# Kernel tuning notes

Hardware: AMD Instinct MI355X
Metric: run time of the kernel (lower is better)

Reference implementation:

```python
import jax, jax.numpy as jnp
import numpy as np

N_HEAD = 16  # matches init_kwargs


def _rope_cos_sin(T, head_dim):
    # inv_freq over even indices, as in AdvancedRotaryEmbedding
    inv_freq = 1.0 / (10000.0 ** (jnp.arange(0, head_dim, 2, dtype=jnp.float32) / head_dim))
    t = jnp.arange(T, dtype=jnp.float32)
    freqs = t[:, None] * inv_freq[None, :]  # [T, head_dim/2]
    return jnp.cos(freqs), jnp.sin(freqs)


def _apply_rope(x, cos, sin):
    # x: [B, H, T, D]; cos/sin: [T, D/2] (broadcast over B, H)
    x1, x2 = x[..., 0::2], x[..., 1::2]
    # half-concat layout, faithful to the module's apply_rotary_emb
    return jnp.concatenate([x1 * cos - x2 * sin, x1 * sin + x2 * cos], axis=-1)


def reference(x, Wq, Wk, Wv, Wo):
    B, T, C = x.shape
    H = N_HEAD
    D = C // H
    # QKV projections (torch Linear: y = x @ W.T), then split heads -> [B, H, T, D]
    q = (x @ Wq.T).reshape(B, T, H, D).transpose(0, 2, 1, 3)
    k = (x @ Wk.T).reshape(B, T, H, D).transpose(0, 2, 1, 3)
    v = (x @ Wv.T).reshape(B, T, H, D).transpose(0, 2, 1, 3)
    cos, sin = _rope_cos_sin(T, D)
    cos = cos.astype(x.dtype)
    sin = sin.astype(x.dtype)
    q = _apply_rope(q, cos, sin)
    k = _apply_rope(k, cos, sin)
    # causal SDPA (eval mode -> dropout_p = 0); jax.nn expects [B, T, H, D]
    y = jax.nn.dot_product_attention(
        q.transpose(0, 2, 1, 3),
        k.transpose(0, 2, 1, 3),
        v.transpose(0, 2, 1, 3),
        is_causal=True,
    )  # [B, T, H, D]
    y = y.reshape(B, T, C)
    return y @ Wo.T


def setup_inputs() -> dict:
    key = jax.random.key(0)
    ks = jax.random.split(key, 5)
    B, T, C = 2, 2048, 1024
    s = 1.0 / np.sqrt(C)
    return {
        "x": jax.random.normal(ks[0], (B, T, C), dtype=jnp.float32),
        "Wq": jax.random.normal(ks[1], (C, C), dtype=jnp.float32) * s,
        "Wk": jax.random.normal(ks[2], (C, C), dtype=jnp.float32) * s,
        "Wv": jax.random.normal(ks[3], (C, C), dtype=jnp.float32) * s,
        "Wo": jax.random.normal(ks[4], (C, C), dtype=jnp.float32) * s,
    }
```

## Files before the change

kernel.cpp:

```cpp
#include <hip/hip_runtime.h>
#include <cstdint>
#include <cstddef>

typedef short s16x8 __attribute__((ext_vector_type(8)));
typedef float f32x4 __attribute__((ext_vector_type(4)));

#define MFMA16(a, b, c) __builtin_amdgcn_mfma_f32_16x16x32_bf16((a), (b), (c), 0, 0, 0)

constexpr int LDP = 72;

__device__ __forceinline__ short f2bf(float f) {
    unsigned u = __builtin_bit_cast(unsigned, f);
    u += 0x7FFFu + ((u >> 16) & 1u);
    return (short)(u >> 16);
}
__device__ __forceinline__ float bf2f(short s) {
    unsigned u = ((unsigned)(unsigned short)s) << 16;
    return __builtin_bit_cast(float, u);
}
__device__ __forceinline__ unsigned pack2(float a, float b) {
    return (unsigned)(unsigned short)f2bf(a) | ((unsigned)(unsigned short)f2bf(b) << 16);
}

__device__ __forceinline__ void async_ld16(const void* g, void* l) {
    __builtin_amdgcn_global_load_lds(
        (const __attribute__((address_space(1))) unsigned int*)g,
        (__attribute__((address_space(3))) unsigned int*)l, 16, 0, 0);
}

__global__ __launch_bounds__(256) void convert_kernel(
    const float* __restrict__ x, const float* __restrict__ Wq,
    const float* __restrict__ Wk, const float* __restrict__ Wv,
    const float* __restrict__ Wo, short* __restrict__ xb, short* __restrict__ wb) {
    const size_t f = ((size_t)blockIdx.x * 256 + threadIdx.x) * 8;
    const float* src;
    short* dst;
    if (f < 4194304) { src = x + f; dst = xb + f; }
    else {
        size_t wo = f - 4194304;
        int seg = (int)(wo >> 20);
        const float* ws4[4] = {Wq, Wk, Wv, Wo};
        src = ws4[seg] + (wo & 1048575u);
        dst = wb + wo;
    }
    float4 a = ((const float4*)src)[0];
    float4 b = ((const float4*)src)[1];
    *(uint4*)dst = make_uint4(pack2(a.x, a.y), pack2(a.z, a.w),
                              pack2(b.x, b.y), pack2(b.z, b.w));
}

__global__ __launch_bounds__(256) void qkv_kernel(
    const short* __restrict__ xb, const short* __restrict__ wb,
    short* __restrict__ Qo, short* __restrict__ Ko, short* __restrict__ VTo) {
    __shared__ __align__(16) short sA[128 * 64];
    __shared__ __align__(16) short sB[128 * 64];
    const int tid = threadIdx.x;
    const int w = tid >> 6, lane = tid & 63, quad = lane >> 4, l15 = lane & 15;
    const int wm = w & 1, wn = w >> 1;
    const int bx = blockIdx.x, by = blockIdx.y;
    const int m0 = by * 128;
    const int nb = bx * 128;

    f32x4 acc[4][4];
#pragma unroll
    for (int i = 0; i < 4; i++)
#pragma unroll
        for (int j = 0; j < 4; j++) acc[i][j] = f32x4{0.f, 0.f, 0.f, 0.f};

    for (int kb = 0; kb < 16; kb++) {
        const int k0 = kb * 64;
        if (kb) __syncthreads();
#pragma unroll
        for (int i = 0; i < 4; i++) {
            int c = i * 256 + tid;
            int row = c >> 3, col8 = (c & 7) * 8;
            async_ld16(xb + (size_t)(m0 + row) * 1024 + k0 + col8,
                       &sA[(i * 256 + w * 64) * 8]);
            async_ld16(wb + (size_t)(nb + row) * 1024 + k0 + col8,
                       &sB[(i * 256 + w * 64) * 8]);
        }
        __syncthreads();
#pragma unroll
        for (int ks = 0; ks < 2; ks++) {
            s16x8 av[4], bv[4];
#pragma unroll
            for (int at = 0; at < 4; at++)
                av[at] = *(const s16x8*)&sA[(wm * 64 + at * 16 + l15) * 64 + ks * 32 + quad * 8];
#pragma unroll
            for (int bt = 0; bt < 4; bt++)
                bv[bt] = *(const s16x8*)&sB[(wn * 64 + bt * 16 + l15) * 64 + ks * 32 + quad * 8];
#pragma unroll
            for (int at = 0; at < 4; at++)
#pragma unroll
                for (int bt = 0; bt < 4; bt++)
                    acc[at][bt] = MFMA16(av[at], bv[bt], acc[at][bt]);
        }
    }

    const int wsel = bx >> 3;
    const int h = (bx & 7) * 2 + wn;
    if (wsel == 2) {
#pragma unroll
        for (int at = 0; at < 4; at++) {
            int m = m0 + wm * 64 + at * 16 + quad * 4;
            int b = m >> 11, t0 = m & 2047;
            size_t base = ((size_t)((b * 16 + h) * 64)) * 2048;
#pragma unroll
            for (int bt = 0; bt < 4; bt++) {
                int d = bt * 16 + l15;
                unsigned lo = pack2(acc[at][bt][0], acc[at][bt][1]);
                unsigned hi = pack2(acc[at][bt][2], acc[at][bt][3]);
                *(uint2*)&VTo[base + (size_t)d * 2048 + t0] = make_uint2(lo, hi);
            }
        }
    } else {
        short* Out = (wsel == 0) ? Qo : Ko;
#pragma unroll
        for (int at = 0; at < 4; at++)
#pragma unroll
            for (int r = 0; r < 4; r++) {
                int m = m0 + wm * 64 + at * 16 + quad * 4 + r;
                int b = m >> 11, t = m & 2047;
                size_t base = (((size_t)(b * 16 + h)) * 2048 + t) * 64;
#pragma unroll
                for (int bt = 0; bt < 4; bt++)
                    Out[base + bt * 16 + l15] = f2bf(acc[at][bt][r]);
            }
    }
}

__global__ __launch_bounds__(256) void rope_kernel(short* __restrict__ Q, short* __restrict__ K) {
    const int rid = blockIdx.x * 256 + threadIdx.x;
    const bool isK = (rid & 65536) != 0;
    short* buf = isK ? K : Q;
    const float sc = isK ? 1.0f : 0.18033688011112042f;
    const int r2 = rid & 65535;
    const int t = r2 & 2047;
    short* row = buf + (size_t)r2 * 64;

    unsigned wv[32];
    const uint4* rp = (const uint4*)row;
#pragma unroll
    for (int c = 0; c < 8; c++) {
        uint4 v = rp[c];
        wv[c * 4 + 0] = v.x; wv[c * 4 + 1] = v.y; wv[c * 4 + 2] = v.z; wv[c * 4 + 3] = v.w;
    }
    float y1[32], y2[32];
    const float tf = (float)t;
#pragma unroll
    for (int i = 0; i < 32; i++) {
        float x1 = bf2f((short)(wv[i] & 0xFFFFu));
        float x2 = bf2f((short)(wv[i] >> 16));
        float inv = expf(-9.2103403719761836f * (float)i * (1.0f / 32.0f));
        float fr = tf * inv;
        float sn, cs;
        sincosf(fr, &sn, &cs);
        y1[i] = (x1 * cs - x2 * sn) * sc;
        y2[i] = (x1 * sn + x2 * cs) * sc;
    }
    unsigned ow[32];
#pragma unroll
    for (int i = 0; i < 16; i++) ow[i] = pack2(y1[2 * i], y1[2 * i + 1]);
#pragma unroll
    for (int i = 0; i < 16; i++) ow[16 + i] = pack2(y2[2 * i], y2[2 * i + 1]);
    uint4* wp = (uint4*)row;
#pragma unroll
    for (int c = 0; c < 8; c++)
        wp[c] = make_uint4(ow[c * 4 + 0], ow[c * 4 + 1], ow[c * 4 + 2], ow[c * 4 + 3]);
}

__global__ __launch_bounds__(256) void attn_kernel(
    const short* __restrict__ Q, const short* __restrict__ K,
    const short* __restrict__ VT, short* __restrict__ Y) {
    __shared__ __align__(16) short sQP[64 * LDP];
    __shared__ __align__(16) short sK[64 * LDP];
    __shared__ __align__(16) short sVT[64 * LDP];

    const int tid = threadIdx.x;
    const int w = tid >> 6, lane = tid & 63, quad = lane >> 4, l15 = lane & 15;
    const int px = blockIdx.x;
    const int bh = blockIdx.y;
    const int b = bh >> 4, h = bh & 15;
    const short* Qp = Q + (size_t)bh * 2048 * 64;
    const short* Kp = K + (size_t)bh * 2048 * 64;
    const short* Vp = VT + (size_t)bh * 64 * 2048;

    for (int pass = 0; pass < 2; pass++) {
        const int qt = pass ? (31 - px) : px;
        __syncthreads();
#pragma unroll
        for (int i = 0; i < 2; i++) {
            int p = tid + i * 256;
            int row = p >> 3, c8 = p & 7;
            uint4 v = *(const uint4*)(Qp + (size_t)(qt * 64 + row) * 64 + c8 * 8);
            *(uint4*)&sQP[row * LDP + c8 * 8] = v;
        }
        __syncthreads();
        s16x8 aq[2];
#pragma unroll
        for (int ks = 0; ks < 2; ks++)
            aq[ks] = *(const s16x8*)&sQP[(w * 16 + l15) * LDP + ks * 32 + quad * 8];

        f32x4 o[4];
#pragma unroll
        for (int i = 0; i < 4; i++) o[i] = f32x4{0.f, 0.f, 0.f, 0.f};
        float mrun = -INFINITY;
        float lrun = 0.f;
        const int q_idx = qt * 64 + w * 16 + l15;

        for (int kt = 0; kt <= qt; kt++) {
            __syncthreads();
#pragma unroll
            for (int i = 0; i < 2; i++) {
                int p = tid + i * 256;
                int row = p >> 3, c8 = p & 7;
                uint4 kv = *(const uint4*)(Kp + (size_t)(kt * 64 + row) * 64 + c8 * 8);
                *(uint4*)&sK[row * LDP + c8 * 8] = kv;
                uint4 vv = *(const uint4*)(Vp + (size_t)row * 2048 + kt * 64 + c8 * 8);
                *(uint4*)&sVT[row * LDP + c8 * 8] = vv;
            }
            __syncthreads();

            f32x4 sa[4];
#pragma unroll
            for (int i = 0; i < 4; i++) sa[i] = f32x4{0.f, 0.f, 0.f, 0.f};
#pragma unroll
            for (int ks = 0; ks < 2; ks++) {
#pragma unroll
                for (int ct = 0; ct < 4; ct++) {
                    s16x8 kf = *(const s16x8*)&sK[(ct * 16 + l15) * LDP + ks * 32 + quad * 8];
                    sa[ct] = MFMA16(kf, aq[ks], sa[ct]);
                }
            }

            const bool diag = (kt == qt);
            float ps[4][4];
#pragma unroll
            for (int ct = 0; ct < 4; ct++) {
                int kbase = kt * 64 + ct * 16 + quad * 4;
#pragma unroll
                for (int r = 0; r < 4; r++) {
                    float s = sa[ct][r];
                    if (diag && (kbase + r) > q_idx) s = -INFINITY;
                    ps[ct][r] = s;
                }
            }
            float cm[4];
#pragma unroll
            for (int ct = 0; ct < 4; ct++)
                cm[ct] = fmaxf(fmaxf(ps[ct][0], ps[ct][1]), fmaxf(ps[ct][2], ps[ct][3]));
            float mx = fmaxf(fmaxf(cm[0], cm[1]), fmaxf(cm[2], cm[3]));
            mx = fmaxf(mx, __shfl_xor(mx, 16));
            mx = fmaxf(mx, __shfl_xor(mx, 32));
            float mnew = fmaxf(mrun, mx);
            float alpha = exp2f(mrun - mnew);
            mrun = mnew;
            float cs[4];
#pragma unroll
            for (int ct = 0; ct < 4; ct++) {
#pragma unroll
                for (int r = 0; r < 4; r++) ps[ct][r] = exp2f(ps[ct][r] - mnew);
                cs[ct] = (ps[ct][0] + ps[ct][1]) + (ps[ct][2] + ps[ct][3]);
            }
            float psum = (cs[0] + cs[1]) + (cs[2] + cs[3]);
            psum += __shfl_xor(psum, 16);
            psum += __shfl_xor(psum, 32);
            lrun = lrun * alpha + psum;

            float arow[4];
#pragma unroll
            for (int r = 0; r < 4; r++) arow[r] = __shfl(alpha, quad * 4 + r);
#pragma unroll
            for (int ct = 0; ct < 4; ct++)
#pragma unroll
                for (int r = 0; r < 4; r++) o[ct][r] *= arow[r];

#pragma unroll
            for (int ct = 0; ct < 4; ct++) {
                unsigned lo = pack2(ps[ct][0], ps[ct][1]);
                unsigned hi = pack2(ps[ct][2], ps[ct][3]);
                *(uint2*)&sQP[(w * 16 + l15) * LDP + ct * 16 + quad * 4] = make_uint2(lo, hi);
            }

#pragma unroll
            for (int ks2 = 0; ks2 < 2; ks2++) {
                s16x8 pa = *(const s16x8*)&sQP[(w * 16 + l15) * LDP + ks2 * 32 + quad * 8];
#pragma unroll
                for (int ct = 0; ct < 4; ct++) {
                    s16x8 vb = *(const s16x8*)&sVT[(ct * 16 + l15) * LDP + ks2 * 32 + quad * 8];
                    o[ct] = MFMA16(pa, vb, o[ct]);
                }
            }
        }

#pragma unroll
        for (int r = 0; r < 4; r++) {
            float linv = 1.0f / __shfl(lrun, quad * 4 + r);
            int t = qt * 64 + w * 16 + quad * 4 + r;
#pragma unroll
            for (int ct = 0; ct < 4; ct++) {
                float val = o[ct][r] * linv;
                Y[((size_t)(b * 2048 + t)) * 1024 + h * 64 + ct * 16 + l15] = f2bf(val);
            }
        }
    }
}

__global__ __launch_bounds__(256) void oproj_kernel(
    const short* __restrict__ Yb, const short* __restrict__ Wob, float* __restrict__ out) {
    __shared__ __align__(16) short sA[128 * 64];
    __shared__ __align__(16) short sB[128 * 64];
    const int tid = threadIdx.x;
    const int w = tid >> 6, lane = tid & 63, quad = lane >> 4, l15 = lane & 15;
    const int wm = w & 1, wn = w >> 1;
    const int m0 = blockIdx.y * 128;
    const int nb = blockIdx.x * 128;

    f32x4 acc[4][4];
#pragma unroll
    for (int i = 0; i < 4; i++)
#pragma unroll
        for (int j = 0; j < 4; j++) acc[i][j] = f32x4{0.f, 0.f, 0.f, 0.f};

    for (int kb = 0; kb < 16; kb++) {
        const int k0 = kb * 64;
        if (kb) __syncthreads();
#pragma unroll
        for (int i = 0; i < 4; i++) {
            int c = i * 256 + tid;
            int row = c >> 3, col8 = (c & 7) * 8;
            async_ld16(Yb + (size_t)(m0 + row) * 1024 + k0 + col8,
                       &sA[(i * 256 + w * 64) * 8]);
            async_ld16(Wob + (size_t)(nb + row) * 1024 + k0 + col8,
                       &sB[(i * 256 + w * 64) * 8]);
        }
        __syncthreads();
#pragma unroll
        for (int ks = 0; ks < 2; ks++) {
            s16x8 av[4], bv[4];
#pragma unroll
            for (int at = 0; at < 4; at++)
                av[at] = *(const s16x8*)&sA[(wm * 64 + at * 16 + l15) * 64 + ks * 32 + quad * 8];
#pragma unroll
            for (int bt = 0; bt < 4; bt++)
                bv[bt] = *(const s16x8*)&sB[(wn * 64 + bt * 16 + l15) * 64 + ks * 32 + quad * 8];
#pragma unroll
            for (int at = 0; at < 4; at++)
#pragma unroll
                for (int bt = 0; bt < 4; bt++)
                    acc[at][bt] = MFMA16(av[at], bv[bt], acc[at][bt]);
        }
    }
#pragma unroll
    for (int at = 0; at < 4; at++)
#pragma unroll
        for (int r = 0; r < 4; r++) {
            int m = m0 + wm * 64 + at * 16 + quad * 4 + r;
#pragma unroll
            for (int bt = 0; bt < 4; bt++) {
                int n = nb + wn * 64 + bt * 16 + l15;
                out[(size_t)m * 1024 + n] = acc[at][bt][r];
            }
        }
}

extern "C" void kernel_launch(void* const* d_in, const int* in_sizes, int n_in,
                              void* d_out, int out_size, void* d_ws, size_t ws_size,
                              hipStream_t stream) {
    (void)in_sizes; (void)n_in; (void)out_size; (void)ws_size;
    const float* x  = (const float*)d_in[0];
    const float* Wq = (const float*)d_in[1];
    const float* Wk = (const float*)d_in[2];
    const float* Wv = (const float*)d_in[3];
    const float* Wo = (const float*)d_in[4];
    float* out = (float*)d_out;

    const size_t NE = (size_t)2 * 16 * 2048 * 64;
    short* Q  = (short*)d_ws;
    short* K  = Q + NE;
    short* VT = K + NE;
    short* Y  = VT + NE;
    short* xb = Y;
    short* wb = Y + NE;

    convert_kernel<<<4096, 256, 0, stream>>>(x, Wq, Wk, Wv, Wo, xb, wb);
    qkv_kernel<<<dim3(24, 32), 256, 0, stream>>>(xb, wb, Q, K, VT);
    rope_kernel<<<512, 256, 0, stream>>>(Q, K);
    attn_kernel<<<dim3(16, 32), 256, 0, stream>>>(Q, K, VT, Y);
    oproj_kernel<<<dim3(8, 32), 256, 0, stream>>>(Y, wb + 3 * 1048576, out);
}
```

Baseline: 237.3 us.

## Split causal attention KV range into chunks with a separate combine kernel

Attention work is split so each block handles one query tile over a chunk of up to eight key tiles. The grid grows from 512 to 2560 blocks, ordered longest-first. Each block writes an unnormalized partial output plus its running max and sum, and a new combine kernel merges them with log-sum-exp rescaling. This is meant to raise occupancy and balance on the many CUs, at the cost of an extra kernel launch and partial-result traffic. The P-to-bf16 pack also switches to truncation instead of round-to-nearest.

Result: faster. 217.7 us (-8.2%).

```diff
diff --git a/kernel.cpp b/kernel.cpp
--- a/kernel.cpp
+++ b/kernel.cpp
@@ -20,6 +20,11 @@
 }
 __device__ __forceinline__ unsigned pack2(float a, float b) {
     return (unsigned)(unsigned short)f2bf(a) | ((unsigned)(unsigned short)f2bf(b) << 16);
+}
+__device__ __forceinline__ unsigned pack2t(float a, float b) {
+    unsigned ua = __builtin_bit_cast(unsigned, a);
+    unsigned ub = __builtin_bit_cast(unsigned, b);
+    return (ua >> 16) | (ub & 0xFFFF0000u);
 }
 
 __device__ __forceinline__ void async_ld16(const void* g, void* l) {
@@ -171,139 +176,198 @@
 
 __global__ __launch_bounds__(256) void attn_kernel(
     const short* __restrict__ Q, const short* __restrict__ K,
-    const short* __restrict__ VT, short* __restrict__ Y) {
+    const short* __restrict__ VT, short* __restrict__ paO, float* __restrict__ ml) {
     __shared__ __align__(16) short sQP[64 * LDP];
     __shared__ __align__(16) short sK[64 * LDP];
     __shared__ __align__(16) short sVT[64 * LDP];
 
     const int tid = threadIdx.x;
     const int w = tid >> 6, lane = tid & 63, quad = lane >> 4, l15 = lane & 15;
-    const int px = blockIdx.x;
+    const int u = 79 - blockIdx.x;
     const int bh = blockIdx.y;
-    const int b = bh >> 4, h = bh & 15;
+
+    int qt, c;
+    if (u < 8)       { qt = u; c = 0; }
+    else if (u < 24) { int v = u - 8;  qt = 8 + (v >> 1); c = v & 1; }
+    else if (u < 48) { int v = u - 24; qt = 16 + v / 3;   c = v - 3 * (qt - 16); }
+    else             { int v = u - 48; qt = 24 + (v >> 2); c = v & 3; }
+    const int kt0 = c * 8;
+    const int kt1 = min(kt0 + 7, qt);
+
     const short* Qp = Q + (size_t)bh * 2048 * 64;
     const short* Kp = K + (size_t)bh * 2048 * 64;
     const short* Vp = VT + (size_t)bh * 64 * 2048;
 
-    for (int pass = 0; pass < 2; pass++) {
-        const int qt = pass ? (31 - px) : px;
+#pragma unroll
+    for (int i = 0; i < 2; i++) {
+        int p = tid + i * 256;
+        int row = p >> 3, c8 = p & 7;
+        uint4 v = *(const uint4*)(Qp + (size_t)(qt * 64 + row) * 64 + c8 * 8);
+        *(uint4*)&sQP[row * LDP + c8 * 8] = v;
+    }
+    __syncthreads();
+    s16x8 aq[2];
+#pragma unroll
+    for (int ks = 0; ks < 2; ks++)
+        aq[ks] = *(const s16x8*)&sQP[(w * 16 + l15) * LDP + ks * 32 + quad * 8];
+
+    f32x4 o[4];
+#pragma unroll
+    for (int i = 0; i < 4; i++) o[i] = f32x4{0.f, 0.f, 0.f, 0.f};
+    float mrun = -INFINITY;
+    float lrun = 0.f;
+    const int q_idx = qt * 64 + w * 16 + l15;
+
+    for (int kt = kt0; kt <= kt1; kt++) {
         __syncthreads();
 #pragma unroll
         for (int i = 0; i < 2; i++) {
             int p = tid + i * 256;
             int row = p >> 3, c8 = p & 7;
-            uint4 v = *(const uint4*)(Qp + (size_t)(qt * 64 + row) * 64 + c8 * 8);
-            *(uint4*)&sQP[row * LDP + c8 * 8] = v;
+            uint4 kv = *(const uint4*)(Kp + (size_t)(kt * 64 + row) * 64 + c8 * 8);
+            *(uint4*)&sK[row * LDP + c8 * 8] = kv;
+            uint4 vv = *(const uint4*)(Vp + (size_t)row * 2048 + kt * 64 + c8 * 8);
+            *(uint4*)&sVT[row * LDP + c8 * 8] = vv;
         }
         __syncthreads();
-        s16x8 aq[2];
-#pragma unroll
-        for (int ks = 0; ks < 2; ks++)
-            aq[ks] = *(const s16x8*)&sQP[(w * 16 + l15) * LDP + ks * 32 + quad * 8];
-
-        f32x4 o[4];
-#pragma unroll
-        for (int i = 0; i < 4; i++) o[i] = f32x4{0.f, 0.f, 0.f, 0.f};
-        float mrun = -INFINITY;
-        float lrun = 0.f;
-        const int q_idx = qt * 64 + w * 16 + l15;
-
-        for (int kt = 0; kt <= qt; kt++) {
-            __syncthreads();
-#pragma unroll
-            for (int i = 0; i < 2; i++) {
-                int p = tid + i * 256;
-                int row = p >> 3, c8 = p & 7;
-                uint4 kv = *(const uint4*)(Kp + (size_t)(kt * 64 + row) * 64 + c8 * 8);
-                *(uint4*)&sK[row * LDP + c8 * 8] = kv;
-                uint4 vv = *(const uint4*)(Vp + (size_t)row * 2048 + kt * 64 + c8 * 8);
-                *(uint4*)&sVT[row * LDP + c8 * 8] = vv;
-            }
-            __syncthreads();
-
-            f32x4 sa[4];
-#pragma unroll
-            for (int i = 0; i < 4; i++) sa[i] = f32x4{0.f, 0.f, 0.f, 0.f};
-#pragma unroll
-            for (int ks = 0; ks < 2; ks++) {
-#pragma unroll
-                for (int ct = 0; ct < 4; ct++) {
-                    s16x8 kf = *(const s16x8*)&sK[(ct * 16 + l15) * LDP + ks * 32 + quad * 8];
-                    sa[ct] = MFMA16(kf, aq[ks], sa[ct]);
-                }
-            }
-
-            const bool diag = (kt == qt);
-            float ps[4][4];
+
+        f32x4 sa[4];
+#pragma unroll
+        for (int i = 0; i < 4; i++) sa[i] = f32x4{0.f, 0.f, 0.f, 0.f};
+#pragma unroll
+        for (int ks = 0; ks < 2; ks++) {
 #pragma unroll
             for (int ct = 0; ct < 4; ct++) {
-                int kbase = kt * 64 + ct * 16 + quad * 4;
-#pragma unroll
-                for (int r = 0; r < 4; r++) {
-                    float s = sa[ct][r];
-                    if (diag && (kbase + r) > q_idx) s = -INFINITY;
-                    ps[ct][r] = s;
-                }
-            }
-            float cm[4];
-#pragma unroll
-            for (int ct = 0; ct < 4; ct++)
-                cm[ct] = fmaxf(fmaxf(ps[ct][0], ps[ct][1]), fmaxf(ps[ct][2], ps[ct][3]));
-            float mx = fmaxf(fmaxf(cm[0], cm[1]), fmaxf(cm[2], cm[3]));
-            mx = fmaxf(mx, __shfl_xor(mx, 16));
-            mx = fmaxf(mx, __shfl_xor(mx, 32));
-            float mnew = fmaxf(mrun, mx);
-            float alpha = exp2f(mrun - mnew);
-            mrun = mnew;
-            float cs[4];
+                s16x8 kf = *(const s16x8*)&sK[(ct * 16 + l15) * LDP + ks * 32 + quad * 8];
+                sa[ct] = MFMA16(kf, aq[ks], sa[ct]);
+            }
+        }
+
+        const bool diag = (kt == qt);
+        float ps[4][4];
+#pragma unroll
+        for (int ct = 0; ct < 4; ct++) {
+            int kbase = kt * 64 + ct * 16 + quad * 4;
+#pragma unroll
+            for (int r = 0; r < 4; r++) {
+                float s = sa[ct][r];
+                if (diag && (kbase + r) > q_idx) s = -INFINITY;
+                ps[ct][r] = s;
+            }
+        }
+        float cm[4];
+#pragma unroll
+        for (int ct = 0; ct < 4; ct++)
+            cm[ct] = fmaxf(fmaxf(ps[ct][0], ps[ct][1]), fmaxf(ps[ct][2], ps[ct][3]));
+        float mx = fmaxf(fmaxf(cm[0], cm[1]), fmaxf(cm[2], cm[3]));
+        mx = fmaxf(mx, __shfl_xor(mx, 16));
+        mx = fmaxf(mx, __shfl_xor(mx, 32));
+        float mnew = fmaxf(mrun, mx);
+        float alpha = exp2f(mrun - mnew);
+        mrun = mnew;
+        float cs[4];
+#pragma unroll
+        for (int ct = 0; ct < 4; ct++) {
+#pragma unroll
+            for (int r = 0; r < 4; r++) ps[ct][r] = exp2f(ps[ct][r] - mnew);
+            cs[ct] = (ps[ct][0] + ps[ct][1]) + (ps[ct][2] + ps[ct][3]);
+        }
+        float psum = (cs[0] + cs[1]) + (cs[2] + cs[3]);
+        psum += __shfl_xor(psum, 16);
+        psum += __shfl_xor(psum, 32);
+        lrun = lrun * alpha + psum;
+
+        float arow[4];
+#pragma unroll
+        for (int r = 0; r < 4; r++) arow[r] = __shfl(alpha, quad * 4 + r);
+#pragma unroll
+        for (int ct = 0; ct < 4; ct++)
+#pragma unroll
+            for (int r = 0; r < 4; r++) o[ct][r] *= arow[r];
+
+#pragma unroll
+        for (int ct = 0; ct < 4; ct++) {
+            unsigned lo = pack2t(ps[ct][0], ps[ct][1]);
+            unsigned hi = pack2t(ps[ct][2], ps[ct][3]);
+            *(uint2*)&sQP[(w * 16 + l15) * LDP + ct * 16 + quad * 4] = make_uint2(lo, hi);
+        }
+
+#pragma unroll
+        for (int ks2 = 0; ks2 < 2; ks2++) {
+            s16x8 pa = *(const s16x8*)&sQP[(w * 16 + l15) * LDP + ks2 * 32 + quad * 8];
 #pragma unroll
             for (int ct = 0; ct < 4; ct++) {
-#pragma unroll
-                for (int r = 0; r < 4; r++) ps[ct][r] = exp2f(ps[ct][r] - mnew);
-                cs[ct] = (ps[ct][0] + ps[ct][1]) + (ps[ct][2] + ps[ct][3]);
-            }
-            float psum = (cs[0] + cs[1]) + (cs[2] + cs[3]);
-            psum += __shfl_xor(psum, 16);
-            psum += __shfl_xor(psum, 32);
-            lrun = lrun * alpha + psum;
-
-            float arow[4];
-#pragma unroll
-            for (int r = 0; r < 4; r++) arow[r] = __shfl(alpha, quad * 4 + r);
-#pragma unroll
-            for (int ct = 0; ct < 4; ct++)
-#pragma unroll
-                for (int r = 0; r < 4; r++) o[ct][r] *= arow[r];
-
-#pragma unroll
-            for (int ct = 0; ct < 4; ct++) {
-                unsigned lo = pack2(ps[ct][0], ps[ct][1]);
-                unsigned hi = pack2(ps[ct][2], ps[ct][3]);
-                *(uint2*)&sQP[(w * 16 + l15) * LDP + ct * 16 + quad * 4] = make_uint2(lo, hi);
-            }
-
-#pragma unroll
-            for (int ks2 = 0; ks2 < 2; ks2++) {
-                s16x8 pa = *(const s16x8*)&sQP[(w * 16 + l15) * LDP + ks2 * 32 + quad * 8];
-#pragma unroll
-                for (int ct = 0; ct < 4; ct++) {
-                    s16x8 vb = *(const s16x8*)&sVT[(ct * 16 + l15) * LDP + ks2 * 32 + quad * 8];
-                    o[ct] = MFMA16(pa, vb, o[ct]);
-                }
-            }
-        }
-
-#pragma unroll
-        for (int r = 0; r < 4; r++) {
-            float linv = 1.0f / __shfl(lrun, quad * 4 + r);
-            int t = qt * 64 + w * 16 + quad * 4 + r;
-#pragma unroll
-            for (int ct = 0; ct < 4; ct++) {
-                float val = o[ct][r] * linv;
-                Y[((size_t)(b * 2048 + t)) * 1024 + h * 64 + ct * 16 + l15] = f2bf(val);
-            }
-        }
-    }
+                s16x8 vb = *(const s16x8*)&sVT[(ct * 16 + l15) * LDP + ks2 * 32 + quad * 8];
+                o[ct] = MFMA16(pa, vb, o[ct]);
+            }
+        }
+    }
+
+    const size_t pbase = ((size_t)(bh * 80 + u)) * 4096;
+#pragma unroll
+    for (int r = 0; r < 4; r++) {
+        int row = w * 16 + quad * 4 + r;
+#pragma unroll
+        for (int ct = 0; ct < 4; ct++)
+            paO[pbase + row * 64 + ct * 16 + l15] = f2bf(o[ct][r]);
+    }
+    if (quad == 0) {
+        int mlbase = (bh * 80 + u) * 128;
+        ml[mlbase + w * 16 + l15] = mrun;
+        ml[mlbase + 64 + w * 16 + l15] = lrun;
+    }
+}
+
+__global__ __launch_bounds__(256) void combine_kernel(
+    const short* __restrict__ paO, const float* __restrict__ ml, short* __restrict__ Y) {
+    const int qt = blockIdx.x, bh = blockIdx.y;
+    const int b = bh >> 4, h = bh & 15;
+    const int nch = (qt >> 3) + 1;
+    int base;
+    if (qt < 8) base = qt;
+    else if (qt < 16) base = 8 + 2 * (qt - 8);
+    else if (qt < 24) base = 24 + 3 * (qt - 16);
+    else base = 48 + 4 * (qt - 24);
+
+    const int row = threadIdx.x >> 2;
+    const int cq = (threadIdx.x & 3) * 16;
+
+    float mi[4], li[4];
+    float M = -INFINITY;
+    for (int i = 0; i < nch; i++) {
+        int mlbase = (bh * 80 + base + i) * 128;
+        mi[i] = ml[mlbase + row];
+        li[i] = ml[mlbase + 64 + row];
+        M = fmaxf(M, mi[i]);
+    }
+    float L = 0.f, ai[4];
+    for (int i = 0; i < nch; i++) {
+        ai[i] = exp2f(mi[i] - M);
+        L += li[i] * ai[i];
+    }
+    const float inv = 1.0f / L;
+
+    float acc[16];
+#pragma unroll
+    for (int j = 0; j < 16; j++) acc[j] = 0.f;
+    for (int i = 0; i < nch; i++) {
+        const short* p = paO + ((size_t)(bh * 80 + base + i)) * 4096 + row * 64 + cq;
+        uint4 v0 = ((const uint4*)p)[0];
+        uint4 v1 = ((const uint4*)p)[1];
+        unsigned vs[8] = {v0.x, v0.y, v0.z, v0.w, v1.x, v1.y, v1.z, v1.w};
+#pragma unroll
+        for (int j = 0; j < 8; j++) {
+            acc[2 * j + 0] += bf2f((short)(vs[j] & 0xFFFFu)) * ai[i];
+            acc[2 * j + 1] += bf2f((short)(vs[j] >> 16)) * ai[i];
+        }
+    }
+    const int t = qt * 64 + row;
+    short* yp = Y + ((size_t)(b * 2048 + t)) * 1024 + h * 64 + cq;
+    unsigned ow[8];
+#pragma unroll
+    for (int j = 0; j < 8; j++) ow[j] = pack2(acc[2 * j] * inv, acc[2 * j + 1] * inv);
+    ((uint4*)yp)[0] = make_uint4(ow[0], ow[1], ow[2], ow[3]);
+    ((uint4*)yp)[1] = make_uint4(ow[4], ow[5], ow[6], ow[7]);
 }
 
 __global__ __launch_bounds__(256) void oproj_kernel(
@@ -376,16 +440,19 @@
     float* out = (float*)d_out;
 
     const size_t NE = (size_t)2 * 16 * 2048 * 64;
-    short* Q  = (short*)d_ws;
-    short* K  = Q + NE;
-    short* VT = K + NE;
-    short* Y  = VT + NE;
-    short* xb = Y;
-    short* wb = Y + NE;
+    short* Q   = (short*)d_ws;
+    short* K   = Q + NE;
+    short* VT  = K + NE;
+    short* Y   = VT + NE;
+    short* xb  = Y;
+    short* wb  = Y + NE;
+    short* paO = wb + NE;
+    float* ml  = (float*)(paO + (size_t)32 * 80 * 4096);
 
     convert_kernel<<<4096, 256, 0, stream>>>(x, Wq, Wk, Wv, Wo, xb, wb);
     qkv_kernel<<<dim3(24, 32), 256, 0, stream>>>(xb, wb, Q, K, VT);
     rope_kernel<<<512, 256, 0, stream>>>(Q, K);
-    attn_kernel<<<dim3(16, 32), 256, 0, stream>>>(Q, K, VT, Y);
+    attn_kernel<<<dim3(80, 32), 256, 0, stream>>>(Q, K, VT, paO, ml);
+    combine_kernel<<<dim3(32, 32), 256, 0, stream>>>(paO, ml, Y);
     oproj_kernel<<<dim3(8, 32), 256, 0, stream>>>(Y, wb + 3 * 1048576, out);
 }
```
